# Kernel tuning notes

Hardware: AMD Instinct MI355X
Metric: run time of the kernel (lower is better)

## Reference

```python
import jax, jax.numpy as jnp
import numpy as np

LAMBDA_OTDL = 1.0


def _emd2_1d(p, q):
    """Exact EMD^2 (squared-distance cost on integer grid) between two 1D
    histograms p, q of length D. For convex cost |i-j|^2 on a line the optimal
    plan is the monotone (quantile) coupling, so
      EMD2 = int_0^1 (F_p^{-1}(t) - F_q^{-1}(t))^2 dt,
    matching ot.emd2 with M[i,j] = |i-j|^2 exactly."""
    D = p.shape[0]
    cp = jnp.cumsum(p)
    cq = jnp.cumsum(q)
    t = jnp.sort(jnp.concatenate([cp, cq]))          # [2D] merged CDF breakpoints
    dt = jnp.diff(t, prepend=jnp.zeros((1,), t.dtype))
    tm = t - 0.5 * dt                                 # segment midpoints
    ip = jnp.clip(jnp.searchsorted(cp, tm, side='left'), 0, D - 1)
    iq = jnp.clip(jnp.searchsorted(cq, tm, side='left'), 0, D - 1)
    return jnp.sum(dt * (ip - iq).astype(p.dtype) ** 2)


def setup_inputs() -> dict:
    key = jax.random.key(0)
    k1, k2 = jax.random.split(key)
    B, C, D, W = 65536, 1, 256, 1
    P = jax.random.uniform(k1, (B, C, D, W), dtype=jnp.float32)
    Q = jax.random.uniform(k2, (B, C, D, W), dtype=jnp.float32)
    return {"P": P, "Q": Q}


def reference(P, Q):
    B = P.shape[0]
    P_prime = P / jnp.sum(P, axis=(2, 3), keepdims=True)
    Q_prime = Q / jnp.sum(Q, axis=(2, 3), keepdims=True)
    p_flat = P_prime.reshape(B, -1)   # [B, D] since C=W=1
    q_flat = Q_prime.reshape(B, -1)
    OT_values = jax.vmap(_emd2_1d)(p_flat, q_flat)          # [B]
    OT_values = jax.lax.stop_gradient(OT_values)            # original detaches (numpy solver)
    mse_loss = jnp.mean((P - Q) ** 2, axis=(1, 2, 3))       # [B]
    loss = mse_loss + LAMBDA_OTDL * OT_values
    return jnp.mean(loss)
```

## Files before the change

### kernel.cpp

```cpp
#include <hip/hip_runtime.h>


#define NW    4
#define DSZ   256
#define LROW  264

template <int CTRL, int RMASK, bool BC>
__device__ __forceinline__ float dpp_add(float x) {
    int t = __builtin_amdgcn_update_dpp(0, __float_as_int(x), CTRL, RMASK, 0xf, BC);
    return x + __int_as_float(t);
}

__device__ __forceinline__ float wave_scan(float x) {
    x = dpp_add<0x111, 0xf, true >(x);
    x = dpp_add<0x112, 0xf, true >(x);
    x = dpp_add<0x114, 0xf, true >(x);
    x = dpp_add<0x118, 0xf, true >(x);
    x = dpp_add<0x142, 0xa, false>(x);
    x = dpp_add<0x143, 0xc, false>(x);
    return x;
}

__device__ __forceinline__ float lane63(float x) {
    return __int_as_float(__builtin_amdgcn_readlane(__float_as_int(x), 63));
}

__global__ __launch_bounds__(256, 8) void otdl_main(
    const float* __restrict__ P, const float* __restrict__ Q,
    double* __restrict__ partial, int B, int bpw)
{
    __shared__ float  s_cp[NW][LROW];
    __shared__ float  s_cq[NW][LROW];
    __shared__ double s_bsum[NW];

    const int tid  = threadIdx.x;
    const int wv   = tid >> 6;
    const int lane = tid & 63;
    const int wgl  = blockIdx.x * NW + wv;

    float* cp = s_cp[wv];
    float* cq = s_cq[wv];

    if (lane == 0) { cp[DSZ] = 2.0f; cq[DSZ] = 2.0f; }

    double acc = 0.0;
    const int  k0      = lane * 8;
    const long rowbase = (long)wgl * bpw;

    float4 pv, qv, npv, nqv;
    {
        long c = (rowbase < B) ? rowbase : (B - 1);
        pv = reinterpret_cast<const float4*>(P + c * DSZ)[lane];
        qv = reinterpret_cast<const float4*>(Q + c * DSZ)[lane];
    }

    for (int it = 0; it < bpw; ++it) {
        long b = rowbase + it;

        if (it + 1 < bpw) {
            long c = (b + 1 < B) ? (b + 1) : (B - 1);
            npv = reinterpret_cast<const float4*>(P + c * DSZ)[lane];
            nqv = reinterpret_cast<const float4*>(Q + c * DSZ)[lane];
        }

        float dx = pv.x - qv.x, dy = pv.y - qv.y;
        float dz = pv.z - qv.z, dw = pv.w - qv.w;
        float msel = dx*dx + dy*dy + dz*dz + dw*dw;

        float pl = pv.x + pv.y + pv.z + pv.w;
        float ql = qv.x + qv.y + qv.z + qv.w;
        float ps = wave_scan(pl);
        float qs = wave_scan(ql);

        float rp = 1.0f / lane63(ps);
        float rq = 1.0f / lane63(qs);
        float pe = ps - pl;
        float qe = qs - ql;

        float vP0 = (pe + pv.x) * rp;
        float vP1 = (pe + pv.x + pv.y) * rp;
        float vP2 = (pe + pv.x + pv.y + pv.z) * rp;
        float vP3 = ps * rp;
        float vQ0 = (qe + qv.x) * rq;
        float vQ1 = (qe + qv.x + qv.y) * rq;
        float vQ2 = (qe + qv.x + qv.y + qv.z) * rq;
        float vQ3 = qs * rq;

        asm volatile("s_waitcnt lgkmcnt(0)" ::: "memory");

        *reinterpret_cast<float4*>(&cp[lane * 4]) = make_float4(vP0, vP1, vP2, vP3);
        *reinterpret_cast<float4*>(&cq[lane * 4]) = make_float4(vQ0, vQ1, vQ2, vQ3);

        asm volatile("s_waitcnt lgkmcnt(0)" ::: "memory");

        int lo = k0 > DSZ ? k0 - DSZ : 0;
        int hi = k0 < DSZ ? k0 : DSZ;
#pragma unroll
        for (int s = 0; s < 9; ++s) {
            int mid = (lo + hi) >> 1;
            int jm1 = k0 - 1 - mid;
            int jr  = jm1 < 0 ? 0 : jm1;
            float cqv = cq[jr];
            float cpv = cp[mid];
            bool pred = (jm1 < 0) || (cqv <= cpv);
            hi = pred ? mid : hi;
            lo = pred ? lo  : mid + 1;
        }
        const float* pA = cp + lo;
        const float* pB = cq + (k0 - lo);

        float u  = (float)(4 * lo - 2 * k0 - 1);
        float a  = pA[0];
        float b2 = pB[0];
        float an = pA[1];
        float bn = pB[1];
        float e_ = 0.0f;
#pragma unroll
        for (int s = 0; s < 8; ++s) {
            bool  ea   = a < b2;
            float val  = ea ? a : b2;
            float u2   = u + 2.0f;
            float coef = ea ? -u2 : u;
            bool  last = ea ? (an == 2.0f) : (bn == 2.0f);
            coef = last ? 0.0f : coef;
            e_ = fmaf(val, coef, e_);
            u  = ea ? u2 : (u - 2.0f);
            pA += ea ? 1 : 0;
            pB += ea ? 0 : 1;
            a  = ea ? an : a;
            b2 = ea ? b2 : bn;
            an = pA[1];
            bn = pB[1];
        }

        if (b < B) acc += (double)(e_ + msel * (1.0f / 256.0f));
        pv = npv;
        qv = nqv;
    }

#pragma unroll
    for (int off = 32; off; off >>= 1) {
        double o = __shfl_xor(acc, off, 64);
        acc += o;
    }
    if (lane == 0) s_bsum[wv] = acc;
    __syncthreads();
    if (tid == 0) {
        partial[blockIdx.x] = s_bsum[0] + s_bsum[1] + s_bsum[2] + s_bsum[3];
    }
}

__global__ __launch_bounds__(256) void otdl_reduce(
    const double* __restrict__ partial, int n, float* __restrict__ out, double invB)
{
    __shared__ double sdata[256];
    double a = 0.0;
    for (int i = threadIdx.x; i < n; i += 256) a += partial[i];
    sdata[threadIdx.x] = a;
    __syncthreads();
    for (int s2 = 128; s2 > 0; s2 >>= 1) {
        if (threadIdx.x < s2) sdata[threadIdx.x] += sdata[threadIdx.x + s2];
        __syncthreads();
    }
    if (threadIdx.x == 0) out[0] = (float)(sdata[0] * invB);
}

extern "C" void kernel_launch(void* const* d_in, const int* in_sizes, int n_in,
                              void* d_out, int out_size, void* d_ws, size_t ws_size,
                              hipStream_t stream)
{
    const float* P = (const float*)d_in[0];
    const float* Q = (const float*)d_in[1];
    float* out = (float*)d_out;
    double* partial = (double*)d_ws;

    int B = in_sizes[0] / DSZ;
    const int blocks = 2048;
    const int totalWaves = blocks * NW;
    int bpw = (B + totalWaves - 1) / totalWaves;

    otdl_main<<<blocks, 256, 0, stream>>>(P, Q, partial, B, bpw);
    otdl_reduce<<<1, 256, 0, stream>>>(partial, blocks, out, 1.0 / (double)B);
}
```

Measured before the change: 47.19 us.

## Process two rows per iteration with double-buffered LDS to interleave dependency chains

The per-wave loop now handles two batch rows per iteration, each with its own LDS buffer. The two independent scans, binary searches and merge walks are interleaved to hide LDS latency and give more instruction-level parallelism. Prefetch of the next pair is moved after the LDS writes, and launch bounds drop to 4 waves per EU to allow more registers. The loop assumes bpw is even (it is 2 with 2048 blocks and B=65536); an odd bpw would silently drop the last row.

```diff
diff --git a/kernel.cpp b/kernel.cpp
--- a/kernel.cpp
+++ b/kernel.cpp
@@ -25,12 +25,12 @@
     return __int_as_float(__builtin_amdgcn_readlane(__float_as_int(x), 63));
 }
 
-__global__ __launch_bounds__(256, 8) void otdl_main(
+__global__ __launch_bounds__(256, 4) void otdl_main(
     const float* __restrict__ P, const float* __restrict__ Q,
     double* __restrict__ partial, int B, int bpw)
 {
-    __shared__ float  s_cp[NW][LROW];
-    __shared__ float  s_cq[NW][LROW];
+    __shared__ float  s_cp[NW][2][LROW];
+    __shared__ float  s_cq[NW][2][LROW];
     __shared__ double s_bsum[NW];
 
     const int tid  = threadIdx.x;
@@ -38,104 +38,153 @@
     const int lane = tid & 63;
     const int wgl  = blockIdx.x * NW + wv;
 
-    float* cp = s_cp[wv];
-    float* cq = s_cq[wv];
-
-    if (lane == 0) { cp[DSZ] = 2.0f; cq[DSZ] = 2.0f; }
+    float* cpA = s_cp[wv][0];
+    float* cqA = s_cq[wv][0];
+    float* cpB = s_cp[wv][1];
+    float* cqB = s_cq[wv][1];
+
+    if (lane == 0) {
+        cpA[DSZ] = 2.0f; cqA[DSZ] = 2.0f;
+        cpB[DSZ] = 2.0f; cqB[DSZ] = 2.0f;
+    }
 
     double acc = 0.0;
     const int  k0      = lane * 8;
+    const int  npair   = bpw >> 1;
     const long rowbase = (long)wgl * bpw;
 
-    float4 pv, qv, npv, nqv;
+    float4 pv0, qv0, pv1, qv1, np0, nq0, np1, nq1;
     {
-        long c = (rowbase < B) ? rowbase : (B - 1);
-        pv = reinterpret_cast<const float4*>(P + c * DSZ)[lane];
-        qv = reinterpret_cast<const float4*>(Q + c * DSZ)[lane];
-    }
-
-    for (int it = 0; it < bpw; ++it) {
-        long b = rowbase + it;
-
-        if (it + 1 < bpw) {
-            long c = (b + 1 < B) ? (b + 1) : (B - 1);
-            npv = reinterpret_cast<const float4*>(P + c * DSZ)[lane];
-            nqv = reinterpret_cast<const float4*>(Q + c * DSZ)[lane];
+        long c0 = (rowbase     < B) ? rowbase     : (B - 1);
+        long c1 = (rowbase + 1 < B) ? rowbase + 1 : (B - 1);
+        pv0 = reinterpret_cast<const float4*>(P + c0 * DSZ)[lane];
+        qv0 = reinterpret_cast<const float4*>(Q + c0 * DSZ)[lane];
+        pv1 = reinterpret_cast<const float4*>(P + c1 * DSZ)[lane];
+        qv1 = reinterpret_cast<const float4*>(Q + c1 * DSZ)[lane];
+    }
+
+    for (int p = 0; p < npair; ++p) {
+        long b = rowbase + 2 * p;
+
+        float dx0 = pv0.x - qv0.x, dy0 = pv0.y - qv0.y;
+        float dz0 = pv0.z - qv0.z, dw0 = pv0.w - qv0.w;
+        float msel0 = dx0*dx0 + dy0*dy0 + dz0*dz0 + dw0*dw0;
+        float dx1 = pv1.x - qv1.x, dy1 = pv1.y - qv1.y;
+        float dz1 = pv1.z - qv1.z, dw1 = pv1.w - qv1.w;
+        float msel1 = dx1*dx1 + dy1*dy1 + dz1*dz1 + dw1*dw1;
+
+        float pl0 = pv0.x + pv0.y + pv0.z + pv0.w;
+        float ql0 = qv0.x + qv0.y + qv0.z + qv0.w;
+        float pl1 = pv1.x + pv1.y + pv1.z + pv1.w;
+        float ql1 = qv1.x + qv1.y + qv1.z + qv1.w;
+
+        float ps0 = wave_scan(pl0);
+        float qs0 = wave_scan(ql0);
+        float ps1 = wave_scan(pl1);
+        float qs1 = wave_scan(ql1);
+
+        float rp0 = 1.0f / lane63(ps0);
+        float rq0 = 1.0f / lane63(qs0);
+        float rp1 = 1.0f / lane63(ps1);
+        float rq1 = 1.0f / lane63(qs1);
+        float pe0 = ps0 - pl0, qe0 = qs0 - ql0;
+        float pe1 = ps1 - pl1, qe1 = qs1 - ql1;
+
+        float4 wP0 = make_float4((pe0 + pv0.x) * rp0,
+                                 (pe0 + pv0.x + pv0.y) * rp0,
+                                 (pe0 + pv0.x + pv0.y + pv0.z) * rp0,
+                                 ps0 * rp0);
+        float4 wQ0 = make_float4((qe0 + qv0.x) * rq0,
+                                 (qe0 + qv0.x + qv0.y) * rq0,
+                                 (qe0 + qv0.x + qv0.y + qv0.z) * rq0,
+                                 qs0 * rq0);
+        float4 wP1 = make_float4((pe1 + pv1.x) * rp1,
+                                 (pe1 + pv1.x + pv1.y) * rp1,
+                                 (pe1 + pv1.x + pv1.y + pv1.z) * rp1,
+                                 ps1 * rp1);
+        float4 wQ1 = make_float4((qe1 + qv1.x) * rq1,
+                                 (qe1 + qv1.x + qv1.y) * rq1,
+                                 (qe1 + qv1.x + qv1.y + qv1.z) * rq1,
+                                 qs1 * rq1);
+
+        asm volatile("s_waitcnt lgkmcnt(0)" ::: "memory");
+
+        *reinterpret_cast<float4*>(&cpA[lane * 4]) = wP0;
+        *reinterpret_cast<float4*>(&cqA[lane * 4]) = wQ0;
+        *reinterpret_cast<float4*>(&cpB[lane * 4]) = wP1;
+        *reinterpret_cast<float4*>(&cqB[lane * 4]) = wQ1;
+
+        asm volatile("s_waitcnt lgkmcnt(0)" ::: "memory");
+
+        if (p + 1 < npair) {
+            long c0 = (b + 2 < B) ? b + 2 : (B - 1);
+            long c1 = (b + 3 < B) ? b + 3 : (B - 1);
+            np0 = reinterpret_cast<const float4*>(P + c0 * DSZ)[lane];
+            nq0 = reinterpret_cast<const float4*>(Q + c0 * DSZ)[lane];
+            np1 = reinterpret_cast<const float4*>(P + c1 * DSZ)[lane];
+            nq1 = reinterpret_cast<const float4*>(Q + c1 * DSZ)[lane];
         }
 
-        float dx = pv.x - qv.x, dy = pv.y - qv.y;
-        float dz = pv.z - qv.z, dw = pv.w - qv.w;
-        float msel = dx*dx + dy*dy + dz*dz + dw*dw;
-
-        float pl = pv.x + pv.y + pv.z + pv.w;
-        float ql = qv.x + qv.y + qv.z + qv.w;
-        float ps = wave_scan(pl);
-        float qs = wave_scan(ql);
-
-        float rp = 1.0f / lane63(ps);
-        float rq = 1.0f / lane63(qs);
-        float pe = ps - pl;
-        float qe = qs - ql;
-
-        float vP0 = (pe + pv.x) * rp;
-        float vP1 = (pe + pv.x + pv.y) * rp;
-        float vP2 = (pe + pv.x + pv.y + pv.z) * rp;
-        float vP3 = ps * rp;
-        float vQ0 = (qe + qv.x) * rq;
-        float vQ1 = (qe + qv.x + qv.y) * rq;
-        float vQ2 = (qe + qv.x + qv.y + qv.z) * rq;
-        float vQ3 = qs * rq;
-
-        asm volatile("s_waitcnt lgkmcnt(0)" ::: "memory");
-
-        *reinterpret_cast<float4*>(&cp[lane * 4]) = make_float4(vP0, vP1, vP2, vP3);
-        *reinterpret_cast<float4*>(&cq[lane * 4]) = make_float4(vQ0, vQ1, vQ2, vQ3);
-
-        asm volatile("s_waitcnt lgkmcnt(0)" ::: "memory");
-
-        int lo = k0 > DSZ ? k0 - DSZ : 0;
-        int hi = k0 < DSZ ? k0 : DSZ;
+        int lo0 = k0 > DSZ ? k0 - DSZ : 0;
+        int hi0 = k0 < DSZ ? k0 : DSZ;
+        int lo1 = lo0, hi1 = hi0;
 #pragma unroll
         for (int s = 0; s < 9; ++s) {
-            int mid = (lo + hi) >> 1;
-            int jm1 = k0 - 1 - mid;
-            int jr  = jm1 < 0 ? 0 : jm1;
-            float cqv = cq[jr];
-            float cpv = cp[mid];
-            bool pred = (jm1 < 0) || (cqv <= cpv);
-            hi = pred ? mid : hi;
-            lo = pred ? lo  : mid + 1;
+            int mid0 = (lo0 + hi0) >> 1;
+            int mid1 = (lo1 + hi1) >> 1;
+            int jm0 = k0 - 1 - mid0;
+            int jm1 = k0 - 1 - mid1;
+            int jr0 = jm0 < 0 ? 0 : jm0;
+            int jr1 = jm1 < 0 ? 0 : jm1;
+            float q0 = cqA[jr0];
+            float c0 = cpA[mid0];
+            float q1 = cqB[jr1];
+            float c1 = cpB[mid1];
+            bool pr0 = (jm0 < 0) || (q0 <= c0);
+            bool pr1 = (jm1 < 0) || (q1 <= c1);
+            hi0 = pr0 ? mid0 : hi0;  lo0 = pr0 ? lo0 : mid0 + 1;
+            hi1 = pr1 ? mid1 : hi1;  lo1 = pr1 ? lo1 : mid1 + 1;
         }
-        const float* pA = cp + lo;
-        const float* pB = cq + (k0 - lo);
-
-        float u  = (float)(4 * lo - 2 * k0 - 1);
-        float a  = pA[0];
-        float b2 = pB[0];
-        float an = pA[1];
-        float bn = pB[1];
-        float e_ = 0.0f;
+
+        const float* pA0 = cpA + lo0;
+        const float* pB0 = cqA + (k0 - lo0);
+        const float* pA1 = cpB + lo1;
+        const float* pB1 = cqB + (k0 - lo1);
+        float u0 = (float)(4 * lo0 - 2 * k0 - 1);
+        float u1 = (float)(4 * lo1 - 2 * k0 - 1);
+        float a0 = pA0[0], c0 = pB0[0], an0 = pA0[1], cn0 = pB0[1];
+        float a1 = pA1[0], c1 = pB1[0], an1 = pA1[1], cn1 = pB1[1];
+        float e0 = 0.0f, e1 = 0.0f;
 #pragma unroll
         for (int s = 0; s < 8; ++s) {
-            bool  ea   = a < b2;
-            float val  = ea ? a : b2;
-            float u2   = u + 2.0f;
-            float coef = ea ? -u2 : u;
-            bool  last = ea ? (an == 2.0f) : (bn == 2.0f);
-            coef = last ? 0.0f : coef;
-            e_ = fmaf(val, coef, e_);
-            u  = ea ? u2 : (u - 2.0f);
-            pA += ea ? 1 : 0;
-            pB += ea ? 0 : 1;
-            a  = ea ? an : a;
-            b2 = ea ? b2 : bn;
-            an = pA[1];
-            bn = pB[1];
+            bool  ea0  = a0 < c0;
+            bool  ea1  = a1 < c1;
+            float val0 = ea0 ? a0 : c0;
+            float val1 = ea1 ? a1 : c1;
+            float u20  = u0 + 2.0f;
+            float u21  = u1 + 2.0f;
+            float cf0  = ea0 ? -u20 : u0;
+            float cf1  = ea1 ? -u21 : u1;
+            bool  ls0  = ea0 ? (an0 == 2.0f) : (cn0 == 2.0f);
+            bool  ls1  = ea1 ? (an1 == 2.0f) : (cn1 == 2.0f);
+            cf0 = ls0 ? 0.0f : cf0;
+            cf1 = ls1 ? 0.0f : cf1;
+            e0 = fmaf(val0, cf0, e0);
+            e1 = fmaf(val1, cf1, e1);
+            u0 = ea0 ? u20 : (u0 - 2.0f);
+            u1 = ea1 ? u21 : (u1 - 2.0f);
+            pA0 += ea0 ? 1 : 0;  pB0 += ea0 ? 0 : 1;
+            pA1 += ea1 ? 1 : 0;  pB1 += ea1 ? 0 : 1;
+            a0 = ea0 ? an0 : a0;  c0 = ea0 ? c0 : cn0;
+            a1 = ea1 ? an1 : a1;  c1 = ea1 ? c1 : cn1;
+            an0 = pA0[1];  cn0 = pB0[1];
+            an1 = pA1[1];  cn1 = pB1[1];
         }
 
-        if (b < B) acc += (double)(e_ + msel * (1.0f / 256.0f));
-        pv = npv;
-        qv = nqv;
+        if (b     < B) acc += (double)(e0 + msel0 * (1.0f / 256.0f));
+        if (b + 1 < B) acc += (double)(e1 + msel1 * (1.0f / 256.0f));
+        pv0 = np0; qv0 = nq0;
+        pv1 = np1; qv1 = nq1;
     }
 
 #pragma unroll
```

Measured after the change: 45.22 us. 4.2% less time.

## Double-buffer LDS CDFs and software-pipeline scan with merge-path evaluation

Applied to the files above, without the earlier changes.

Splits each row into a front stage (load, wave scan, normalise, write CDF to LDS) and a merge stage. It double-buffers the per-wave LDS CDF arrays so row r+1's scan can overlap row r's merge search, and drops the explicit lgkmcnt waits. It also swaps the division for the hardware reciprocal and removes the per-step 'last element' check, replacing it with a single correction on lane 63. The hardware reciprocal is less exact, and removing the waits assumes the wave's LDS ordering makes its own writes visible.

```diff
diff --git a/kernel.cpp b/kernel.cpp
--- a/kernel.cpp
+++ b/kernel.cpp
@@ -3,7 +3,7 @@
 
 #define NW    4
 #define DSZ   256
-#define LROW  264
+#define LROW  260
 
 template <int CTRL, int RMASK, bool BC>
 __device__ __forceinline__ float dpp_add(float x) {
@@ -25,12 +25,39 @@
     return __int_as_float(__builtin_amdgcn_readlane(__float_as_int(x), 63));
 }
 
+__device__ __forceinline__ float fe_stage(const float4 pv, const float4 qv,
+                                          float* cp, float* cq, int lane) {
+    float dx = pv.x - qv.x, dy = pv.y - qv.y;
+    float dz = pv.z - qv.z, dw = pv.w - qv.w;
+    float msel = dx*dx + dy*dy + dz*dz + dw*dw;
+
+    float pl = pv.x + pv.y + pv.z + pv.w;
+    float ql = qv.x + qv.y + qv.z + qv.w;
+    float ps = wave_scan(pl);
+    float qs = wave_scan(ql);
+    float rp = __builtin_amdgcn_rcpf(lane63(ps));
+    float rq = __builtin_amdgcn_rcpf(lane63(qs));
+    float pe = ps - pl, qe = qs - ql;
+
+    float4 wP = make_float4((pe + pv.x) * rp,
+                            (pe + pv.x + pv.y) * rp,
+                            (pe + pv.x + pv.y + pv.z) * rp,
+                            ps * rp);
+    float4 wQ = make_float4((qe + qv.x) * rq,
+                            (qe + qv.x + qv.y) * rq,
+                            (qe + qv.x + qv.y + qv.z) * rq,
+                            qs * rq);
+    *reinterpret_cast<float4*>(&cp[lane * 4]) = wP;
+    *reinterpret_cast<float4*>(&cq[lane * 4]) = wQ;
+    return msel;
+}
+
 __global__ __launch_bounds__(256, 8) void otdl_main(
     const float* __restrict__ P, const float* __restrict__ Q,
     double* __restrict__ partial, int B, int bpw)
 {
-    __shared__ float  s_cp[NW][LROW];
-    __shared__ float  s_cq[NW][LROW];
+    __shared__ float  s_cp[NW][2][LROW];
+    __shared__ float  s_cq[NW][2][LROW];
     __shared__ double s_bsum[NW];
 
     const int tid  = threadIdx.x;
@@ -38,77 +65,63 @@
     const int lane = tid & 63;
     const int wgl  = blockIdx.x * NW + wv;
 
-    float* cp = s_cp[wv];
-    float* cq = s_cq[wv];
-
-    if (lane == 0) { cp[DSZ] = 2.0f; cq[DSZ] = 2.0f; }
+    if (lane == 0) {
+        s_cp[wv][0][DSZ] = 2.0f; s_cq[wv][0][DSZ] = 2.0f;
+        s_cp[wv][1][DSZ] = 2.0f; s_cq[wv][1][DSZ] = 2.0f;
+    }
 
     double acc = 0.0;
     const int  k0      = lane * 8;
     const long rowbase = (long)wgl * bpw;
+    const bool is63    = (lane == 63);
 
-    float4 pv, qv, npv, nqv;
+    float4 pv, qv;
     {
         long c = (rowbase < B) ? rowbase : (B - 1);
         pv = reinterpret_cast<const float4*>(P + c * DSZ)[lane];
         qv = reinterpret_cast<const float4*>(Q + c * DSZ)[lane];
     }
 
-    for (int it = 0; it < bpw; ++it) {
-        long b = rowbase + it;
+    float mselC = fe_stage(pv, qv, s_cp[wv][0], s_cq[wv][0], lane);
+    if (bpw > 1) {
+        long c = (rowbase + 1 < B) ? rowbase + 1 : (B - 1);
+        pv = reinterpret_cast<const float4*>(P + c * DSZ)[lane];
+        qv = reinterpret_cast<const float4*>(Q + c * DSZ)[lane];
+    }
 
-        if (it + 1 < bpw) {
-            long c = (b + 1 < B) ? (b + 1) : (B - 1);
-            npv = reinterpret_cast<const float4*>(P + c * DSZ)[lane];
-            nqv = reinterpret_cast<const float4*>(Q + c * DSZ)[lane];
+#pragma unroll 2
+    for (int r = 0; r < bpw; ++r) {
+        const int cur = r & 1;
+
+        float mselN = 0.0f;
+        if (r + 1 < bpw) {
+            mselN = fe_stage(pv, qv, s_cp[wv][cur ^ 1], s_cq[wv][cur ^ 1], lane);
+        }
+        if (r + 2 < bpw) {
+            long c = (rowbase + r + 2 < B) ? rowbase + r + 2 : (B - 1);
+            pv = reinterpret_cast<const float4*>(P + c * DSZ)[lane];
+            qv = reinterpret_cast<const float4*>(Q + c * DSZ)[lane];
         }
 
-        float dx = pv.x - qv.x, dy = pv.y - qv.y;
-        float dz = pv.z - qv.z, dw = pv.w - qv.w;
-        float msel = dx*dx + dy*dy + dz*dz + dw*dw;
-
-        float pl = pv.x + pv.y + pv.z + pv.w;
-        float ql = qv.x + qv.y + qv.z + qv.w;
-        float ps = wave_scan(pl);
-        float qs = wave_scan(ql);
-
-        float rp = 1.0f / lane63(ps);
-        float rq = 1.0f / lane63(qs);
-        float pe = ps - pl;
-        float qe = qs - ql;
-
-        float vP0 = (pe + pv.x) * rp;
-        float vP1 = (pe + pv.x + pv.y) * rp;
-        float vP2 = (pe + pv.x + pv.y + pv.z) * rp;
-        float vP3 = ps * rp;
-        float vQ0 = (qe + qv.x) * rq;
-        float vQ1 = (qe + qv.x + qv.y) * rq;
-        float vQ2 = (qe + qv.x + qv.y + qv.z) * rq;
-        float vQ3 = qs * rq;
-
-        asm volatile("s_waitcnt lgkmcnt(0)" ::: "memory");
-
-        *reinterpret_cast<float4*>(&cp[lane * 4]) = make_float4(vP0, vP1, vP2, vP3);
-        *reinterpret_cast<float4*>(&cq[lane * 4]) = make_float4(vQ0, vQ1, vQ2, vQ3);
-
-        asm volatile("s_waitcnt lgkmcnt(0)" ::: "memory");
+        const float* cp = s_cp[wv][cur];
+        const float* cq = s_cq[wv][cur];
 
         int lo = k0 > DSZ ? k0 - DSZ : 0;
         int hi = k0 < DSZ ? k0 : DSZ;
 #pragma unroll
         for (int s = 0; s < 9; ++s) {
             int mid = (lo + hi) >> 1;
-            int jm1 = k0 - 1 - mid;
-            int jr  = jm1 < 0 ? 0 : jm1;
-            float cqv = cq[jr];
-            float cpv = cp[mid];
-            bool pred = (jm1 < 0) || (cqv <= cpv);
+            int jm  = k0 - 1 - mid;
+            int jr  = jm < 0 ? 0 : jm;
+            float qv_ = cq[jr];
+            float cv_ = cp[mid];
+            bool pred = (jm < 0) || (qv_ <= cv_);
             hi = pred ? mid : hi;
             lo = pred ? lo  : mid + 1;
         }
+
         const float* pA = cp + lo;
         const float* pB = cq + (k0 - lo);
-
         float u  = (float)(4 * lo - 2 * k0 - 1);
         float a  = pA[0];
         float b2 = pB[0];
@@ -121,8 +134,6 @@
             float val  = ea ? a : b2;
             float u2   = u + 2.0f;
             float coef = ea ? -u2 : u;
-            bool  last = ea ? (an == 2.0f) : (bn == 2.0f);
-            coef = last ? 0.0f : coef;
             e_ = fmaf(val, coef, e_);
             u  = ea ? u2 : (u - 2.0f);
             pA += ea ? 1 : 0;
@@ -133,9 +144,10 @@
             bn = pB[1];
         }
 
-        if (b < B) acc += (double)(e_ + msel * (1.0f / 256.0f));
-        pv = npv;
-        qv = nqv;
+        e_ -= is63 ? fabsf(cp[DSZ - 1] - cq[DSZ - 1]) : 0.0f;
+
+        if (rowbase + r < B) acc += (double)(e_ + mselC * (1.0f / 256.0f));
+        mselC = mselN;
     }
 
 #pragma unroll
```

Result: faster. 41.41 us (-12.2%).
